# Kernel tuning notes

Hardware: AMD Instinct MI355X
Metric: run time of the kernel (lower is better)

## Reference

```python
import jax, jax.numpy as jnp
import numpy as np

B = 4      # cfg.TRAIN.IMS_PER_BATCH
P = 256    # proposals per image (equal per image; all labels > 0)
C = 151    # cfg.MODEL.NUM_CLASSES
R = 51     # cfg.MODEL.NUM_RELATIONS
W = 0.5    # cfg.REL_INFER.NONE_BGREL_WEIGHT


def setup_inputs() -> dict:
    key = jax.random.key(0)
    k1, k2, k3, k4 = jax.random.split(key, 4)
    roi_scores = jax.random.normal(k1, (B * P, C), dtype=jnp.float32)
    rel_scores = jax.random.normal(k2, (B * P * P, R), dtype=jnp.float32)
    roi_labels = jax.random.randint(k3, (B * P,), 1, C, dtype=jnp.int32)  # labels > 0 (fg only)
    # sparse relation co-occurrence matrix densified; background relation slice set to 1
    relationship_mat = (jax.random.uniform(k4, (C, C, R)) < 0.05).astype(jnp.float32)
    relationship_mat = relationship_mat.at[:, :, 0].set(1.0)
    return {
        "roi_scores": roi_scores,
        "rel_scores": rel_scores,
        "relationship_mat": relationship_mat,
        "roi_labels": roi_labels,
        "num_images": B,
    }


def reference(roi_scores, rel_scores, relationship_mat, roi_labels, num_images):
    nb = num_images
    p = roi_scores.shape[0] // nb
    rel = rel_scores.reshape(nb, p, p, -1)          # [B, P, P, R]
    labels = roi_labels.reshape(nb, p)              # [B, P]
    # computed in the original forward but unused by the returned loss
    _unary = jax.nn.log_softmax(roi_scores, axis=1)
    off_diag = (1.0 - jnp.eye(p, dtype=roi_scores.dtype))  # zero out p == q pairs

    def per_image(lab, rl):
        # lab: [P] int, rl: [P, P, R]
        A = relationship_mat[lab]        # [P, C, R]  rows gathered by subject label
        At = relationship_mat[:, lab]    # [C, P, R]  cols gathered by subject label
        # b[p,q,c] = A[p,c,0]*rl[p,q,0] + W * sum_{r>=1} A[p,c,r]*rl[p,q,r]
        b = A[:, None, :, 0] * rl[:, :, None, 0] \
            + W * jnp.einsum('pcr,pqr->pqc', A[..., 1:], rl[..., 1:])
        # t[p,q,c] = At[c,p,0]*rl[q,p,0] + W * sum_{r>=1} At[c,p,r]*rl[q,p,r]
        t = At[..., 0].T[:, None, :] * rl[..., 0].T[:, :, None] \
            + W * jnp.einsum('cpr,qpr->pqc', At[..., 1:], rl[..., 1:])
        theta = 0.5 * (b + t) * off_diag[:, :, None]  # mask diagonal pairs
        theta = theta.sum(0)                          # sum over partner p -> [P, C]
        logp = jax.nn.log_softmax(theta, axis=1)
        return -logp[jnp.arange(p), lab]              # [P]

    loss = jax.vmap(per_image)(labels, rel)           # [B, P]
    return loss.mean()
```

## Files before the change

### kernel.cpp

```cpp
#include <hip/hip_runtime.h>
#include <math.h>

#define NB 4
#define PP 256
#define CC 151
#define RR 51
#define CM 160
#define KI 64
#define ML (CC*KI)
#define KS 64
#define NROW (NB*PP)
#define RELTOT (NB*PP*PP*RR)
#define ALIM (RELTOT - 8)

typedef _Float16 half8 __attribute__((ext_vector_type(8)));
typedef float floatx4 __attribute__((ext_vector_type(4)));

#define OFF_M1 ((size_t)0)
#define OFF_M2 (OFF_M1 + (size_t)CM*ML*2)
#define OFF_PT (OFF_M2 + (size_t)CM*ML*2)

__global__ __launch_bounds__(256) void prep_kernel(const float* __restrict__ M,
                                                   _Float16* __restrict__ m1,
                                                   _Float16* __restrict__ m2,
                                                   float* __restrict__ out) {
    const int c = blockIdx.x;
    const int mat = blockIdx.y;
    if (c == 0 && mat == 0 && threadIdx.x == 0) *out = 0.f;
    _Float16* dst = (mat ? m2 : m1) + (size_t)c * ML;
    for (int e = threadIdx.x; e < ML; e += 256) {
        int l = e >> 6, r = e & 63;
        float v = 0.f;
        if (r < RR && c < CC) {
            size_t src = ((size_t)(mat ? c * CC + l : l * CC + c)) * RR + r;
            v = (r == 0 ? 0.5f : 0.25f) * M[src];
        }
        dst[e] = (_Float16)v;
    }
}

__global__ __launch_bounds__(256) void gemm_kernel(const float* __restrict__ rel,
                                                   const _Float16* __restrict__ m1,
                                                   const _Float16* __restrict__ m2,
                                                   const int* __restrict__ labels,
                                                   float* __restrict__ part) {
    __shared__ _Float16 Bt[2][640 * 8];
    const int tid  = threadIdx.x;
    const int ks   = blockIdx.x & 63;
    const int rbk  = (blockIdx.x >> 6) & 3;
    const int n    = blockIdx.x >> 8;
    const int wave = tid >> 6, lane = tid & 63;
    const int m16  = lane & 15, quad = lane >> 4;
    const int i0   = ks * 4;
    const int qimg = rbk * 64 + wave * 16 + m16;

    int labs[4];
    #pragma unroll
    for (int j = 0; j < 4; ++j) labs[j] = labels[n * PP + i0 + j];

    floatx4 acc[10];
    #pragma unroll
    for (int ct = 0; ct < 10; ++ct) acc[ct] = (floatx4){0.f, 0.f, 0.f, 0.f};

    auto stageB = [&](int h, int buf) {
        const int ii = h >> 2, mh = (h >> 1) & 1, half = h & 1;
        const _Float16* base = mh ? m2 : m1;
        const int lab = labs[ii];
        #pragma unroll
        for (int j = 0; j < 3; ++j) {
            int s = j * 256 + tid;
            if (s < 640) {
                int oct = s / 160;
                int c = s - oct * 160;
                const _Float16* g = base + (size_t)c * ML + lab * KI + half * 32 + oct * 8;
                __builtin_amdgcn_global_load_lds(
                    (const __attribute__((address_space(1))) unsigned int*)g,
                    (__attribute__((address_space(3))) unsigned int*)(&Bt[buf][(size_t)s * 8]),
                    16, 0, 0);
            }
        }
    };
    auto loadA = [&](int h, float* v) {
        const int ii = h >> 2, mh = (h >> 1) & 1, half = h & 1;
        const int i = i0 + ii;
        int idx = mh ? ((n * PP + qimg) * PP + i) * RR + half * 32 + quad * 8
                     : ((n * PP + i) * PP + qimg) * RR + half * 32 + quad * 8;
        idx = min(idx, ALIM);
        const float* p = rel + idx;
        #pragma unroll
        for (int j = 0; j < 8; ++j) v[j] = p[j];
    };

    stageB(0, 0);
    float av[8];
    loadA(0, av);

    #pragma unroll
    for (int h = 0; h < 16; ++h) {
        __syncthreads();
        if (h < 15) stageB(h + 1, (h + 1) & 1);
        float avn[8];
        if (h < 15) loadA(h + 1, avn);

        const bool dz = (i0 + (h >> 2)) == qimg;
        half8 a;
        #pragma unroll
        for (int j = 0; j < 8; ++j) a[j] = (_Float16)(dz ? 0.f : av[j]);

        const _Float16* bb = &Bt[h & 1][((size_t)quad * 160 + m16) * 8];
        #pragma unroll
        for (int ct = 0; ct < 10; ++ct) {
            half8 b = *(const half8*)(bb + ct * 128);
            acc[ct] = __builtin_amdgcn_mfma_f32_16x16x32_f16(a, b, acc[ct], 0, 0, 0);
        }
        #pragma unroll
        for (int j = 0; j < 8; ++j) av[j] = avn[j];
    }

    float* pb = part + ((size_t)ks * NROW + n * PP + rbk * 64 + wave * 16) * CM;
    #pragma unroll
    for (int ct = 0; ct < 10; ++ct)
        #pragma unroll
        for (int reg = 0; reg < 4; ++reg)
            pb[(size_t)(quad * 4 + reg) * CM + ct * 16 + m16] = acc[ct][reg];
}

__global__ __launch_bounds__(256) void reduce_loss_kernel(const float* __restrict__ part,
                                                          const int* __restrict__ labels,
                                                          float* __restrict__ out) {
    __shared__ float th[CM];
    const int row = blockIdx.x;
    const int t = threadIdx.x;
    if (t < CM) {
        float s = 0.f;
        #pragma unroll
        for (int ks = 0; ks < KS; ++ks)
            s += part[((size_t)ks * NROW + row) * CM + t];
        th[t] = s;
    }
    __syncthreads();
    if (t < 64) {
        float v0 = (t < CC)       ? th[t]       : -INFINITY;
        float v1 = (t + 64 < CC)  ? th[t + 64]  : -INFINITY;
        float v2 = (t + 128 < CC) ? th[t + 128] : -INFINITY;
        float m = fmaxf(v0, fmaxf(v1, v2));
        #pragma unroll
        for (int o = 32; o > 0; o >>= 1) m = fmaxf(m, __shfl_xor(m, o, 64));
        float s = 0.f;
        if (t < CC)       s += expf(v0 - m);
        if (t + 64 < CC)  s += expf(v1 - m);
        if (t + 128 < CC) s += expf(v2 - m);
        #pragma unroll
        for (int o = 32; o > 0; o >>= 1) s += __shfl_xor(s, o, 64);
        if (t == 0) {
            atomicAdd(out, (m + logf(s) - th[labels[row]]) * (1.0f / NROW));
        }
    }
}

extern "C" void kernel_launch(void* const* d_in, const int* in_sizes, int n_in,
                              void* d_out, int out_size, void* d_ws, size_t ws_size,
                              hipStream_t stream) {
    const float* rel    = (const float*)d_in[1];
    const float* relmat = (const float*)d_in[2];
    const int*   labels = (const int*)d_in[3];
    float* out = (float*)d_out;
    char* ws = (char*)d_ws;

    _Float16* m1 = (_Float16*)(ws + OFF_M1);
    _Float16* m2 = (_Float16*)(ws + OFF_M2);
    float*  part = (float*)(ws + OFF_PT);

    prep_kernel<<<dim3(CM, 2), 256, 0, stream>>>(relmat, m1, m2, out);
    gemm_kernel<<<NB * 4 * KS, 256, 0, stream>>>(rel, m1, m2, labels, part);
    reduce_loss_kernel<<<NROW, 256, 0, stream>>>(part, labels, out);
}
```

Baseline: 183.7 us.

## Switch GEMM to 32x32x16 MFMA with label-contiguous B layout

The GEMM now uses 32x32x16 MFMA tiles instead of 16x16x32, so each block covers 128 rows of the image with 5 accumulator tiles of 16 floats, and half as many blocks are launched. The prep kernel rewrites the relationship matrices into a layout where each label's slab is contiguous (per r-octet, per class), so the B staging copies one contiguous chunk per step instead of strided gathers. The K loop now runs 32 steps of 16 instead of 16 steps of 32. This is meant to cut LDS staging traffic and improve MFMA efficiency. In exchange it uses more accumulator registers and fewer blocks, which may lower occupancy.

```diff
diff --git a/kernel.cpp b/kernel.cpp
--- a/kernel.cpp
+++ b/kernel.cpp
@@ -7,29 +7,32 @@
 #define RR 51
 #define CM 160
 #define KI 64
-#define ML (CC*KI)
 #define KS 64
 #define NROW (NB*PP)
 #define RELTOT (NB*PP*PP*RR)
 #define ALIM (RELTOT - 8)
+#define MLB 10240
 
 typedef _Float16 half8 __attribute__((ext_vector_type(8)));
-typedef float floatx4 __attribute__((ext_vector_type(4)));
+typedef float floatx16 __attribute__((ext_vector_type(16)));
 
 #define OFF_M1 ((size_t)0)
-#define OFF_M2 (OFF_M1 + (size_t)CM*ML*2)
-#define OFF_PT (OFF_M2 + (size_t)CM*ML*2)
+#define OFF_M2 (OFF_M1 + (size_t)CC*MLB*2)
+#define OFF_PT (OFF_M2 + (size_t)CC*MLB*2)
 
 __global__ __launch_bounds__(256) void prep_kernel(const float* __restrict__ M,
                                                    _Float16* __restrict__ m1,
                                                    _Float16* __restrict__ m2,
                                                    float* __restrict__ out) {
-    const int c = blockIdx.x;
+    const int l = blockIdx.x;
     const int mat = blockIdx.y;
-    if (c == 0 && mat == 0 && threadIdx.x == 0) *out = 0.f;
-    _Float16* dst = (mat ? m2 : m1) + (size_t)c * ML;
-    for (int e = threadIdx.x; e < ML; e += 256) {
-        int l = e >> 6, r = e & 63;
+    if (l == 0 && mat == 0 && threadIdx.x == 0) *out = 0.f;
+    _Float16* dst = (mat ? m2 : m1) + (size_t)l * MLB;
+    for (int e = threadIdx.x; e < MLB; e += 256) {
+        int oct = e / 1280;
+        int rem = e - oct * 1280;
+        int c = rem >> 3, j = rem & 7;
+        int r = oct * 8 + j;
         float v = 0.f;
         if (r < RR && c < CC) {
             size_t src = ((size_t)(mat ? c * CC + l : l * CC + c)) * RR + r;
@@ -44,47 +47,46 @@
                                                    const _Float16* __restrict__ m2,
                                                    const int* __restrict__ labels,
                                                    float* __restrict__ part) {
-    __shared__ _Float16 Bt[2][640 * 8];
+    __shared__ _Float16 Bt[2][2560];
     const int tid  = threadIdx.x;
     const int ks   = blockIdx.x & 63;
-    const int rbk  = (blockIdx.x >> 6) & 3;
-    const int n    = blockIdx.x >> 8;
+    const int rbk  = (blockIdx.x >> 6) & 1;
+    const int n    = blockIdx.x >> 7;
     const int wave = tid >> 6, lane = tid & 63;
-    const int m16  = lane & 15, quad = lane >> 4;
+    const int m32  = lane & 31, kh = lane >> 5;
     const int i0   = ks * 4;
-    const int qimg = rbk * 64 + wave * 16 + m16;
+    const int rowimg = rbk * 128 + wave * 32 + m32;
 
     int labs[4];
     #pragma unroll
     for (int j = 0; j < 4; ++j) labs[j] = labels[n * PP + i0 + j];
 
-    floatx4 acc[10];
+    floatx16 acc[5];
     #pragma unroll
-    for (int ct = 0; ct < 10; ++ct) acc[ct] = (floatx4){0.f, 0.f, 0.f, 0.f};
+    for (int ct = 0; ct < 5; ++ct)
+        #pragma unroll
+        for (int r2 = 0; r2 < 16; ++r2) acc[ct][r2] = 0.f;
 
     auto stageB = [&](int h, int buf) {
-        const int ii = h >> 2, mh = (h >> 1) & 1, half = h & 1;
-        const _Float16* base = mh ? m2 : m1;
-        const int lab = labs[ii];
+        const int il = h >> 3, mh = (h >> 2) & 1, t = h & 3;
+        const _Float16* base = (mh ? m2 : m1) + (size_t)labs[il] * MLB + t * 2560;
         #pragma unroll
-        for (int j = 0; j < 3; ++j) {
+        for (int j = 0; j < 2; ++j) {
             int s = j * 256 + tid;
-            if (s < 640) {
-                int oct = s / 160;
-                int c = s - oct * 160;
-                const _Float16* g = base + (size_t)c * ML + lab * KI + half * 32 + oct * 8;
+            if (s < 320) {
                 __builtin_amdgcn_global_load_lds(
-                    (const __attribute__((address_space(1))) unsigned int*)g,
+                    (const __attribute__((address_space(1))) unsigned int*)(base + s * 8),
                     (__attribute__((address_space(3))) unsigned int*)(&Bt[buf][(size_t)s * 8]),
                     16, 0, 0);
             }
         }
     };
     auto loadA = [&](int h, float* v) {
-        const int ii = h >> 2, mh = (h >> 1) & 1, half = h & 1;
-        const int i = i0 + ii;
-        int idx = mh ? ((n * PP + qimg) * PP + i) * RR + half * 32 + quad * 8
-                     : ((n * PP + i) * PP + qimg) * RR + half * 32 + quad * 8;
+        const int il = h >> 3, mh = (h >> 2) & 1, t = h & 3;
+        const int i = i0 + il;
+        const int r0 = t * 16 + kh * 8;
+        int idx = mh ? ((n * PP + rowimg) * PP + i) * RR + r0
+                     : ((n * PP + i) * PP + rowimg) * RR + r0;
         idx = min(idx, ALIM);
         const float* p = rel + idx;
         #pragma unroll
@@ -95,34 +97,36 @@
     float av[8];
     loadA(0, av);
 
-    #pragma unroll
-    for (int h = 0; h < 16; ++h) {
+    #pragma unroll 2
+    for (int h = 0; h < 32; ++h) {
         __syncthreads();
-        if (h < 15) stageB(h + 1, (h + 1) & 1);
+        if (h < 31) stageB(h + 1, (h + 1) & 1);
         float avn[8];
-        if (h < 15) loadA(h + 1, avn);
+        if (h < 31) loadA(h + 1, avn);
 
-        const bool dz = (i0 + (h >> 2)) == qimg;
+        const bool dz = (i0 + (h >> 3)) == rowimg;
         half8 a;
         #pragma unroll
         for (int j = 0; j < 8; ++j) a[j] = (_Float16)(dz ? 0.f : av[j]);
 
-        const _Float16* bb = &Bt[h & 1][((size_t)quad * 160 + m16) * 8];
+        const _Float16* bb = &Bt[h & 1][(size_t)(kh * 160 + m32) * 8];
         #pragma unroll
-        for (int ct = 0; ct < 10; ++ct) {
-            half8 b = *(const half8*)(bb + ct * 128);
-            acc[ct] = __builtin_amdgcn_mfma_f32_16x16x32_f16(a, b, acc[ct], 0, 0, 0);
+        for (int ct = 0; ct < 5; ++ct) {
+            half8 b = *(const half8*)(bb + ct * 256);
+            acc[ct] = __builtin_amdgcn_mfma_f32_32x32x16_f16(a, b, acc[ct], 0, 0, 0);
         }
         #pragma unroll
         for (int j = 0; j < 8; ++j) av[j] = avn[j];
     }
 
-    float* pb = part + ((size_t)ks * NROW + n * PP + rbk * 64 + wave * 16) * CM;
+    float* pb = part + ((size_t)ks * NROW + n * PP + rbk * 128 + wave * 32) * CM;
     #pragma unroll
-    for (int ct = 0; ct < 10; ++ct)
+    for (int ct = 0; ct < 5; ++ct)
         #pragma unroll
-        for (int reg = 0; reg < 4; ++reg)
-            pb[(size_t)(quad * 4 + reg) * CM + ct * 16 + m16] = acc[ct][reg];
+        for (int reg = 0; reg < 16; ++reg) {
+            int row = (reg & 3) + 8 * (reg >> 2) + 4 * kh;
+            pb[(size_t)row * CM + ct * 32 + m32] = acc[ct][reg];
+        }
 }
 
 __global__ __launch_bounds__(256) void reduce_loss_kernel(const float* __restrict__ part,
@@ -171,7 +175,7 @@
     _Float16* m2 = (_Float16*)(ws + OFF_M2);
     float*  part = (float*)(ws + OFF_PT);
 
-    prep_kernel<<<dim3(CM, 2), 256, 0, stream>>>(relmat, m1, m2, out);
-    gemm_kernel<<<NB * 4 * KS, 256, 0, stream>>>(rel, m1, m2, labels, part);
+    prep_kernel<<<dim3(CC, 2), 256, 0, stream>>>(relmat, m1, m2, out);
+    gemm_kernel<<<NB * 2 * KS, 256, 0, stream>>>(rel, m1, m2, labels, part);
     reduce_loss_kernel<<<NROW, 256, 0, stream>>>(part, labels, out);
 }
```

After: 166.0 us. 1.11x faster.
